# Kernel tuning notes

Measured on AMD Instinct MI355X. Metric: run time of the kernel, lower is better.

The kernel has to match this reference:

```python
import jax, jax.numpy as jnp
import numpy as np

B, T, E, H, C = 64, 512, 768, 128, 18


def setup_inputs() -> dict:
    key = jax.random.key(0)
    ks = jax.random.split(key, 16)
    s = 1.0 / np.sqrt(H)
    inp = {
        "x": jax.random.normal(ks[0], (B, T, E), jnp.float32),
        "attention_mask": jnp.ones((B, T), jnp.int32),
        "labels": jax.random.randint(ks[1], (B, T), 0, C, jnp.int32),
        "Wih_f": jax.random.uniform(ks[2], (4 * H, E), jnp.float32, -s, s),
        "Whh_f": jax.random.uniform(ks[3], (4 * H, H), jnp.float32, -s, s),
        "b_f": jax.random.uniform(ks[4], (4 * H,), jnp.float32, -s, s),
        "Wih_b": jax.random.uniform(ks[5], (4 * H, E), jnp.float32, -s, s),
        "Whh_b": jax.random.uniform(ks[6], (4 * H, H), jnp.float32, -s, s),
        "b_b": jax.random.uniform(ks[7], (4 * H,), jnp.float32, -s, s),
        "Wfc": jax.random.uniform(ks[8], (C, 2 * H), jnp.float32, -s, s),
        "bfc": jax.random.uniform(ks[9], (C,), jnp.float32, -s, s),
        "start_trans": jax.random.normal(ks[10], (C,), jnp.float32) * 0.1,
        "end_trans": jax.random.normal(ks[11], (C,), jnp.float32) * 0.1,
        "trans": jax.random.normal(ks[12], (C, C), jnp.float32) * 0.1,
    }
    return inp


def _lstm_dir(x, Wih, Whh, b, reverse=False):
    # x: [B, T, E] -> hidden states [B, T, H]; torch LSTM gate order i,f,g,o
    if reverse:
        x = x[:, ::-1]
    pre = jnp.einsum("bte,ge->btg", x, Wih) + b  # [B, T, 4H] input projection once
    h0 = jnp.zeros((x.shape[0], H), x.dtype)

    def step(carry, pt):
        h, c = carry
        g = pt + h @ Whh.T
        i, f, gg, o = jnp.split(g, 4, axis=-1)
        c = jax.nn.sigmoid(f) * c + jax.nn.sigmoid(i) * jnp.tanh(gg)
        h = jax.nn.sigmoid(o) * jnp.tanh(c)
        return (h, c), h

    _, hs = jax.lax.scan(step, (h0, h0), jnp.swapaxes(pre, 0, 1))
    hs = jnp.swapaxes(hs, 0, 1)
    if reverse:
        hs = hs[:, ::-1]
    return hs


def _crf_loglik(em, tags, mask, start, end, trans):
    # pytorch-crf log-likelihood, batch_first. em [B,T,C], tags/mask [B,T]
    b, t, _ = em.shape
    maskf = mask.astype(em.dtype)
    tags = tags.astype(jnp.int32)
    # numerator: score of the given tag path
    em_sc = jnp.take_along_axis(em, tags[..., None], axis=2)[..., 0]  # [B,T]
    num = start[tags[:, 0]] + em_sc[:, 0]
    num = num + jnp.sum(em_sc[:, 1:] * maskf[:, 1:], axis=1)
    num = num + jnp.sum(trans[tags[:, :-1], tags[:, 1:]] * maskf[:, 1:], axis=1)
    last_idx = jnp.sum(mask.astype(jnp.int32), axis=1) - 1
    last_tags = jnp.take_along_axis(tags, last_idx[:, None], axis=1)[:, 0]
    num = num + end[last_tags]
    # denominator: forward algorithm (logsumexp recurrence over time)
    alpha0 = start + em[:, 0]  # [B,C]

    def step(alpha, inp):
        e_t, m_t = inp
        new = jax.scipy.special.logsumexp(alpha[:, :, None] + trans[None], axis=1) + e_t
        return jnp.where(m_t[:, None], new, alpha), None

    alpha, _ = jax.lax.scan(
        step, alpha0,
        (jnp.swapaxes(em[:, 1:], 0, 1), jnp.swapaxes(mask[:, 1:].astype(bool), 0, 1)),
    )
    den = jax.scipy.special.logsumexp(alpha + end, axis=1)
    return num - den


def _viterbi(em, start, end, trans):
    # em [B,T,C] -> best path [B,T] (full mask)
    s0 = start + em[:, 0]

    def fstep(score, e_t):
        cand = score[:, :, None] + trans[None]  # [B,C,C]
        return jnp.max(cand, axis=1) + e_t, jnp.argmax(cand, axis=1)

    score, bptr = jax.lax.scan(fstep, s0, jnp.swapaxes(em[:, 1:], 0, 1))  # bptr [T-1,B,C]
    last = jnp.argmax(score + end, axis=1)  # [B]

    def bstep(tag, ptr_t):
        prev = jnp.take_along_axis(ptr_t, tag[:, None], axis=1)[:, 0]
        return prev, prev

    _, path = jax.lax.scan(bstep, last, bptr, reverse=True)  # [T-1,B]
    return jnp.concatenate([jnp.swapaxes(path, 0, 1), last[:, None]], axis=1)


def reference(x, attention_mask, labels, Wih_f, Whh_f, b_f, Wih_b, Whh_b, b_b,
              Wfc, bfc, start_trans, end_trans, trans):
    hf = _lstm_dir(x, Wih_f, Whh_f, b_f, reverse=False)
    hb = _lstm_dir(x, Wih_b, Whh_b, b_b, reverse=True)
    seq = jnp.concatenate([hf, hb], axis=-1)  # [B,T,2H]
    em = seq @ Wfc.T + bfc  # [B,T,C] emissions
    mask = attention_mask.astype(bool)
    llh = _crf_loglik(em, labels, mask, start_trans, end_trans, trans)
    loss = -jnp.sum(llh) / x.shape[0]  # reduction='sum' then / batch_size
    path = _viterbi(em, start_trans, end_trans, trans) + 1  # res_paths = x+1
    return path, loss
```

## Files before the change

### kernel.cpp

```cpp
#include <hip/hip_runtime.h>
#include <hip/hip_bf16.h>
#include <math.h>

typedef __attribute__((ext_vector_type(8))) short short8;
typedef __attribute__((ext_vector_type(4))) float f32x4;

constexpr int nB = 64, nT = 512, nE = 768, nH = 128, nG = 512, nC = 18;
constexpr int nBT = nB * nT;

__device__ __forceinline__ float bf2f(unsigned short u) { return __uint_as_float(((unsigned int)u) << 16); }
__device__ __forceinline__ unsigned short f2bf(float f) {
  __hip_bfloat16 h = __float2bfloat16(f);
  return *reinterpret_cast<unsigned short*>(&h);
}
__device__ __forceinline__ float rlane(float v, int lane) {
  return __uint_as_float(__builtin_amdgcn_readlane(__float_as_uint(v), lane));
}
__device__ __forceinline__ float fast_sig(float x) {
  return __builtin_amdgcn_rcpf(1.0f + __builtin_amdgcn_exp2f(-1.44269504f * x));
}
__device__ __forceinline__ float fast_tanh(float x) {
  return 1.0f - 2.0f * __builtin_amdgcn_rcpf(1.0f + __builtin_amdgcn_exp2f(2.88539008f * x));
}

__global__ __launch_bounds__(256) void cvt_kernel(const float* __restrict__ in,
                                                  unsigned short* __restrict__ out, int n8) {
  int i = blockIdx.x * blockDim.x + threadIdx.x;
  const int stride = gridDim.x * blockDim.x;
  for (; i < n8; i += stride) {
    const float4 a = ((const float4*)in)[(size_t)i * 2];
    const float4 b = ((const float4*)in)[(size_t)i * 2 + 1];
    unsigned short u[8] = {f2bf(a.x), f2bf(a.y), f2bf(a.z), f2bf(a.w),
                           f2bf(b.x), f2bf(b.y), f2bf(b.z), f2bf(b.w)};
    ((float4*)out)[i] = *(float4*)u;
  }
}

__global__ __launch_bounds__(256) void cvtw_kernel(const float* __restrict__ inF,
                                                   const float* __restrict__ inB,
                                                   unsigned short* __restrict__ outF,
                                                   unsigned short* __restrict__ outB, int n8) {
  const int half = gridDim.x >> 1;
  const float* in = (blockIdx.x < half) ? inF : inB;
  unsigned short* out = (blockIdx.x < half) ? outF : outB;
  const int bid = (blockIdx.x < half) ? blockIdx.x : blockIdx.x - half;
  int i = bid * blockDim.x + threadIdx.x;
  const int stride = half * blockDim.x;
  for (; i < n8; i += stride) {
    const float4 a = ((const float4*)in)[(size_t)i * 2];
    const float4 b = ((const float4*)in)[(size_t)i * 2 + 1];
    unsigned short u[8] = {f2bf(a.x), f2bf(a.y), f2bf(a.z), f2bf(a.w),
                           f2bf(b.x), f2bf(b.y), f2bf(b.z), f2bf(b.w)};
    ((float4*)out)[i] = *(float4*)u;
  }
}

__global__ __launch_bounds__(256) void proj_kernel(
    const unsigned short* __restrict__ xbf,
    const unsigned short* __restrict__ wfb, const unsigned short* __restrict__ wbb,
    const float* __restrict__ biasF, const float* __restrict__ biasB,
    unsigned short* __restrict__ Pf, unsigned short* __restrict__ Pb)
{
  const int bid = blockIdx.x;
  const int mt = bid & 255, sub = bid >> 8;
  const int dir = sub >> 2, nt = sub & 3;
  const unsigned short* W = dir ? wbb : wfb;
  const float* bias = dir ? biasB : biasF;
  unsigned short* P = dir ? Pb : Pf;
  const int m0 = mt * 128, n0 = nt * 128;

  __shared__ unsigned short As[128 * 40];
  __shared__ unsigned short Bs[128 * 40];
  const int tid = threadIdx.x;
  const int w = tid >> 6, lane = tid & 63, l15 = lane & 15, l4 = lane >> 4;
  const int wr = w >> 1, wc = w & 1;
  const int srow = tid >> 1, shalf = tid & 1;

  const unsigned short* srcA = xbf + (size_t)(m0 + srow) * nE + shalf * 16;
  const unsigned short* srcB = W + (size_t)(n0 + srow) * nE + shalf * 16;

  f32x4 acc[4][4];
#pragma unroll
  for (int i = 0; i < 4; ++i)
#pragma unroll
    for (int j = 0; j < 4; ++j) acc[i][j] = (f32x4){0.f, 0.f, 0.f, 0.f};

  for (int k0 = 0; k0 < nE; k0 += 32) {
    const float4 a0 = *(const float4*)(srcA + k0);
    const float4 a1 = *(const float4*)(srcA + k0 + 8);
    const float4 b0 = *(const float4*)(srcB + k0);
    const float4 b1 = *(const float4*)(srcB + k0 + 8);
    __syncthreads();
    *(float4*)&As[srow * 40 + shalf * 16] = a0;
    *(float4*)&As[srow * 40 + shalf * 16 + 8] = a1;
    *(float4*)&Bs[srow * 40 + shalf * 16] = b0;
    *(float4*)&Bs[srow * 40 + shalf * 16 + 8] = b1;
    __syncthreads();
    short8 af[4], bfr[4];
#pragma unroll
    for (int i = 0; i < 4; ++i) af[i] = *(const short8*)&As[(wr * 64 + i * 16 + l15) * 40 + l4 * 8];
#pragma unroll
    for (int j = 0; j < 4; ++j) bfr[j] = *(const short8*)&Bs[(wc * 64 + j * 16 + l15) * 40 + l4 * 8];
#pragma unroll
    for (int i = 0; i < 4; ++i)
#pragma unroll
      for (int j = 0; j < 4; ++j)
        acc[i][j] = __builtin_amdgcn_mfma_f32_16x16x32_bf16(af[i], bfr[j], acc[i][j], 0, 0, 0);
  }
  float bv[4];
#pragma unroll
  for (int j = 0; j < 4; ++j) bv[j] = bias[n0 + wc * 64 + j * 16 + l15];
#pragma unroll
  for (int i = 0; i < 4; ++i) {
#pragma unroll
    for (int j = 0; j < 4; ++j) {
      const int col = n0 + wc * 64 + j * 16 + l15;
#pragma unroll
      for (int r = 0; r < 4; ++r) {
        const int row = m0 + wr * 64 + i * 16 + l4 * 4 + r;
        P[(size_t)row * nG + col] = f2bf(acc[i][j][r] + bv[j]);
      }
    }
  }
}

__global__ __launch_bounds__(512, 1) void lstm_kernel(
    const unsigned short* __restrict__ Pf, const unsigned short* __restrict__ Pb,
    const float* __restrict__ WhhF, const float* __restrict__ WhhB,
    unsigned short* __restrict__ hf, unsigned short* __restrict__ hb)
{
  const int bid = blockIdx.x;
  const int dir = bid & 1, grp = bid >> 1;
  const int b0 = grp * 4;
  const unsigned short* pre = dir ? Pb : Pf;
  const float* Whh = dir ? WhhB : WhhF;
  unsigned short* hout = dir ? hb : hf;

  const int tid = threadIdx.x, w = tid >> 6, lane = tid & 63;
  const int l15 = lane & 15, l4 = lane >> 4;
  const int batch = l15 & 3, msel = l15 >> 2;
  const int cell = w * 16 + msel * 4 + l4;
  const int swz = batch * 40;

  __shared__ unsigned short h_lds[2 * 4 * 128];

  short8 Af[4][4];
#pragma unroll
  for (int m = 0; m < 4; ++m) {
    const int gp = w * 64 + m * 16 + l15;
    const int gorig = (gp & 3) * 128 + (gp >> 2);
#pragma unroll
    for (int kk = 0; kk < 4; ++kk) {
      const float* wp = Whh + (size_t)gorig * nH + kk * 32 + l4 * 8;
      const float4 v0 = *(const float4*)wp;
      const float4 v1 = *(const float4*)(wp + 4);
      unsigned short u[8] = {f2bf(v0.x), f2bf(v0.y), f2bf(v0.z), f2bf(v0.w),
                             f2bf(v1.x), f2bf(v1.y), f2bf(v1.z), f2bf(v1.w)};
      Af[m][kk] = *(short8*)u;
    }
  }
  for (int i = tid; i < 2 * 4 * 128; i += 512) h_lds[i] = 0;

  float c_state = 0.f;
  const unsigned short* pbase = pre + (size_t)(b0 + batch) * nT * nG + cell;

  unsigned short pA[4], pB[4];
  {
    const int tt0 = dir ? (nT - 1) : 0;
    const int tt1 = dir ? (nT - 2) : 1;
#pragma unroll
    for (int r = 0; r < 4; ++r) pA[r] = pbase[(size_t)tt0 * nG + r * 128];
#pragma unroll
    for (int r = 0; r < 4; ++r) pB[r] = pbase[(size_t)tt1 * nG + r * 128];
  }
  __syncthreads();

#define LSTM_STEP(RB, T, BUFC)                                                   \
  {                                                                              \
    const int ttime = dir ? (nT - 1 - (T)) : (T);                                \
    float pg[4];                                                                 \
    _Pragma("unroll")                                                            \
    for (int r = 0; r < 4; ++r) pg[r] = bf2f(BUFC[r]);                           \
    {                                                                            \
      const int tl = ((T) + 2 < nT) ? (T) + 2 : (T);                             \
      const int ttl = dir ? (nT - 1 - tl) : tl;                                  \
      _Pragma("unroll")                                                          \
      for (int r = 0; r < 4; ++r) BUFC[r] = pbase[(size_t)ttl * nG + r * 128];   \
    }                                                                            \
    short8 bfr[4];                                                               \
    _Pragma("unroll")                                                            \
    for (int kk = 0; kk < 4; ++kk) {                                             \
      const int idx = (RB) * 512 + batch * 128 + ((kk * 32 + l4 * 8) ^ swz);     \
      bfr[kk] = *(const short8*)&h_lds[idx];                                     \
    }                                                                            \
    f32x4 acc[4];                                                                \
    _Pragma("unroll")                                                            \
    for (int m = 0; m < 4; ++m) acc[m] = (f32x4){0.f, 0.f, 0.f, 0.f};            \
    _Pragma("unroll")                                                            \
    for (int kk = 0; kk < 4; ++kk)                                               \
      _Pragma("unroll")                                                          \
      for (int m = 0; m < 4; ++m)                                                \
        acc[m] = __builtin_amdgcn_mfma_f32_16x16x32_bf16(Af[m][kk], bfr[kk], acc[m], 0, 0, 0); \
    const float g0 = msel < 2 ? (msel == 0 ? acc[0][0] : acc[1][0]) : (msel == 2 ? acc[2][0] : acc[3][0]); \
    const float g1 = msel < 2 ? (msel == 0 ? acc[0][1] : acc[1][1]) : (msel == 2 ? acc[2][1] : acc[3][1]); \
    const float g2 = msel < 2 ? (msel == 0 ? acc[0][2] : acc[1][2]) : (msel == 2 ? acc[2][2] : acc[3][2]); \
    const float g3 = msel < 2 ? (msel == 0 ? acc[0][3] : acc[1][3]) : (msel == 2 ? acc[2][3] : acc[3][3]); \
    const float gi = g0 + pg[0], gf = g1 + pg[1], gg = g2 + pg[2], go = g3 + pg[3]; \
    c_state = fast_sig(gf) * c_state + fast_sig(gi) * fast_tanh(gg);             \
    const float hval = fast_sig(go) * fast_tanh(c_state);                        \
    const unsigned short hu = f2bf(hval);                                        \
    h_lds[((RB) ^ 1) * 512 + batch * 128 + (cell ^ swz)] = hu;                   \
    hout[((size_t)(b0 + batch) * nT + ttime) * nH + cell] = hu;                  \
    asm volatile("s_waitcnt lgkmcnt(0)" ::: "memory");                           \
    __builtin_amdgcn_sched_barrier(0);                                           \
    __builtin_amdgcn_s_barrier();                                                \
  }

  for (int t2 = 0; t2 < nT; t2 += 2) {
    LSTM_STEP(0, t2, pA)
    LSTM_STEP(1, t2 + 1, pB)
  }
#undef LSTM_STEP
}

__global__ __launch_bounds__(256) void em_kernel(
    const unsigned short* __restrict__ hf, const unsigned short* __restrict__ hb,
    const float* __restrict__ Wfc, const float* __restrict__ bfc,
    float* __restrict__ em)
{
  __shared__ float seq[32][260];
  __shared__ float Wf[18][260];
  const int tid = threadIdx.x;
  const int row0 = blockIdx.x * 32;
  for (int i = tid; i < 32 * 32; i += 256) {
    const int r = i >> 5, seg = i & 31;
    const unsigned short* src = (seg < 16) ? (hf + (size_t)(row0 + r) * nH + seg * 8)
                                           : (hb + (size_t)(row0 + r) * nH + (seg - 16) * 8);
    const float4 v = *(const float4*)src;
    const unsigned short* u = (const unsigned short*)&v;
#pragma unroll
    for (int k = 0; k < 8; ++k) seq[r][seg * 8 + k] = bf2f(u[k]);
  }
  for (int i = tid; i < nC * 256; i += 256) {
    const int cc = i >> 8, k = i & 255;
    Wf[cc][k] = Wfc[cc * 256 + k];
  }
  __syncthreads();
  for (int o = tid; o < 32 * nC; o += 256) {
    const int r = o / nC, cc = o - r * nC;
    float acc = bfc[cc];
    const float4* s4 = (const float4*)&seq[r][0];
    const float4* w4 = (const float4*)&Wf[cc][0];
#pragma unroll
    for (int q = 0; q < 64; ++q) {
      const float4 a = s4[q]; const float4 wv = w4[q];
      acc += a.x * wv.x + a.y * wv.y + a.z * wv.z + a.w * wv.w;
    }
    em[(size_t)(row0 + r) * nC + cc] = acc;
  }
}

__global__ __launch_bounds__(64) void crfvit_kernel(
    const float* __restrict__ em, const int* __restrict__ labels,
    const int* __restrict__ mask, const float* __restrict__ start,
    const float* __restrict__ endt, const float* __restrict__ trans,
    float* __restrict__ llh, float* __restrict__ out_path)
{
  constexpr float K2 = 1.44269504088896f;
  constexpr float LN2 = 0.69314718055995f;
  const int b = blockIdx.x >> 1, role = blockIdx.x & 1;
  const int l = threadIdx.x;
  __shared__ float tr[nC * nC];
  __shared__ unsigned char bp[(nT - 1) * nC];
  __shared__ unsigned char path[nT];
  for (int i = l; i < nC * nC; i += 64) tr[i] = trans[i];
  __syncthreads();
  const float* eb = em + (size_t)b * nT * nC;
  const int lc = l < nC ? l : nC - 1;

#define MAX18(c) fmaxf(fmaxf(fmaxf(fmaxf(fmaxf(c[0], c[1]), c[2]), fmaxf(fmaxf(c[3], c[4]), c[5])),           \
                             fmaxf(fmaxf(fmaxf(c[6], c[7]), c[8]), fmaxf(fmaxf(c[9], c[10]), c[11]))),        \
                       fmaxf(fmaxf(fmaxf(c[12], c[13]), c[14]), fmaxf(fmaxf(c[15], c[16]), c[17])))
#define TREESUM(ex, s) {                                                          \
    const float p0 = ex[0] + ex[1], p1 = ex[2] + ex[3], p2 = ex[4] + ex[5];       \
    const float p3 = ex[6] + ex[7], p4 = ex[8] + ex[9], p5 = ex[10] + ex[11];     \
    const float p6 = ex[12] + ex[13], p7 = ex[14] + ex[15], p8 = ex[16] + ex[17]; \
    const float q0 = p0 + p1, q1 = p2 + p3, q2 = p4 + p5, q3 = p6 + p7;           \
    s = ((q0 + q1) + (q2 + q3)) + p8;                                             \
  }

  if (role == 0) {
    const int* tg = labels + (size_t)b * nT;
    const int* mk = mask + (size_t)b * nT;

    float np = 0.f; int cnt = 0;
    for (int t = l; t < nT; t += 64) {
      const int tag = tg[t];
      const float e = eb[(size_t)t * nC + tag];
      if (t == 0) np += start[tag] + e;
      else np += (float)mk[t] * (e + tr[tg[t - 1] * nC + tag]);
      cnt += mk[t];
    }
#pragma unroll
    for (int off = 32; off; off >>= 1) { np += __shfl_xor(np, off); cnt += __shfl_xor(cnt, off); }
    const float num = np + endt[tg[cnt - 1]];

    float trc[nC];
#pragma unroll
    for (int i = 0; i < nC; ++i) trc[i] = tr[i * nC + lc] * K2;

    float alpha2 = (start[lc] + eb[lc]) * K2;
    float ec[8], en[8];
#pragma unroll
    for (int j = 0; j < 8; ++j) ec[j] = eb[j * nC + lc] * K2;
#pragma unroll
    for (int j = 0; j < 8; ++j) en[j] = eb[(8 + j) * nC + lc] * K2;
    unsigned long long mb = __ballot(mk[l] != 0);

#define CRF_STEP(T, E) {                                                          \
      float cand[nC];                                                             \
      _Pragma("unroll")                                                           \
      for (int i = 0; i < nC; ++i) cand[i] = rlane(alpha2, i) + trc[i];           \
      const float m = MAX18(cand);                                                \
      float ex[nC];                                                               \
      _Pragma("unroll")                                                           \
      for (int i = 0; i < nC; ++i) ex[i] = __builtin_amdgcn_exp2f(cand[i] - m);   \
      float s; TREESUM(ex, s);                                                    \
      const float anew = m + __builtin_amdgcn_logf(s) + (E);                      \
      alpha2 = ((mb >> ((T) & 63)) & 1) ? anew : alpha2;                          \
    }

#pragma unroll
    for (int j = 1; j < 8; ++j) CRF_STEP(j, ec[j])
    for (int c = 1; c < 64; ++c) {
#pragma unroll
      for (int j = 0; j < 8; ++j) ec[j] = en[j];
      const int tn = (c < 63) ? (c + 1) * 8 : 504;
#pragma unroll
      for (int j = 0; j < 8; ++j) en[j] = eb[(size_t)(tn + j) * nC + lc] * K2;
      if ((c & 7) == 0) mb = __ballot(mk[c * 8 + l] != 0);
#pragma unroll
      for (int j = 0; j < 8; ++j) CRF_STEP(c * 8 + j, ec[j])
    }
#undef CRF_STEP
    const float v = (l < nC) ? (alpha2 + endt[l] * K2) : -3.0e38f;
    float m = v;
#pragma unroll
    for (int off = 32; off; off >>= 1) m = fmaxf(m, __shfl_xor(m, off));
    float s = (l < nC) ? __builtin_amdgcn_exp2f(v - m) : 0.f;
#pragma unroll
    for (int off = 32; off; off >>= 1) s += __shfl_xor(s, off);
    if (l == 0) llh[b] = num - (m + __builtin_amdgcn_logf(s)) * LN2;
  } else {
    float trc[nC];
#pragma unroll
    for (int i = 0; i < nC; ++i) trc[i] = tr[i * nC + lc];

    float score_r = start[lc] + eb[lc];
    float ec[8], en[8];
#pragma unroll
    for (int j = 0; j < 8; ++j) ec[j] = eb[j * nC + lc];
#pragma unroll
    for (int j = 0; j < 8; ++j) en[j] = eb[(8 + j) * nC + lc];

#define VIT_STEP(T, E) {                                                          \
      float cand[nC];                                                             \
      _Pragma("unroll")                                                           \
      for (int i = 0; i < nC; ++i) cand[i] = rlane(score_r, i) + trc[i];          \
      const float m = MAX18(cand);                                                \
      int sel[nC];                                                                \
      _Pragma("unroll")                                                           \
      for (int i = 0; i < nC; ++i) sel[i] = (cand[i] == m) ? i : 63;              \
      int arg = sel[0];                                                           \
      _Pragma("unroll")                                                           \
      for (int i = 1; i < nC; ++i) arg = min(arg, sel[i]);                        \
      score_r = m + (E);                                                          \
      if (l < nC) bp[((T) - 1) * nC + l] = (unsigned char)arg;                    \
    }

#pragma unroll
    for (int j = 1; j < 8; ++j) VIT_STEP(j, ec[j])
    for (int c = 1; c < 64; ++c) {
#pragma unroll
      for (int j = 0; j < 8; ++j) ec[j] = en[j];
      const int tn = (c < 63) ? (c + 1) * 8 : 504;
#pragma unroll
      for (int j = 0; j < 8; ++j) en[j] = eb[(size_t)(tn + j) * nC + lc];
#pragma unroll
      for (int j = 0; j < 8; ++j) VIT_STEP(c * 8 + j, ec[j])
    }
#undef VIT_STEP
    if (l == 0) {
      float mm = -3.0e38f; int last = 0;
      for (int i = 0; i < nC; ++i) {
        const float v = rlane(score_r, i) + endt[i];
        if (v > mm) { mm = v; last = i; }
      }
      path[nT - 1] = (unsigned char)last;
      int cur = last;
      for (int t = nT - 2; t >= 0; --t) { cur = bp[t * nC + cur]; path[t] = (unsigned char)cur; }
    }
    asm volatile("s_waitcnt lgkmcnt(0)" ::: "memory");
    __builtin_amdgcn_wave_barrier();
    for (int t = l; t < nT; t += 64) out_path[(size_t)b * nT + t] = (float)(path[t] + 1);
  }
#undef MAX18
#undef TREESUM
}

__global__ __launch_bounds__(64) void loss_kernel(const float* __restrict__ llh, float* __restrict__ out)
{
  const int l = threadIdx.x;
  float v = llh[l];
#pragma unroll
  for (int off = 32; off; off >>= 1) v += __shfl_xor(v, off);
  if (l == 0) out[0] = -v / (float)nB;
}

extern "C" void kernel_launch(void* const* d_in, const int* in_sizes, int n_in,
                              void* d_out, int out_size, void* d_ws, size_t ws_size,
                              hipStream_t stream)
{
  const float* x      = (const float*)d_in[0];
  const int*   amask  = (const int*)d_in[1];
  const int*   labels = (const int*)d_in[2];
  const float* Wih_f  = (const float*)d_in[3];
  const float* Whh_f  = (const float*)d_in[4];
  const float* b_f    = (const float*)d_in[5];
  const float* Wih_b  = (const float*)d_in[6];
  const float* Whh_b  = (const float*)d_in[7];
  const float* b_b    = (const float*)d_in[8];
  const float* Wfc    = (const float*)d_in[9];
  const float* bfc    = (const float*)d_in[10];
  const float* start  = (const float*)d_in[11];
  const float* endt   = (const float*)d_in[12];
  const float* trans  = (const float*)d_in[13];

  float* out = (float*)d_out;
  float* ws = (float*)d_ws;
  unsigned short* preF = (unsigned short*)ws;
  unsigned short* preB = preF + (size_t)nBT * nG;
  unsigned short* hf   = preB + (size_t)nBT * nG;
  unsigned short* hb   = hf + (size_t)nBT * nH;
  float* em  = (float*)(hb + (size_t)nBT * nH);
  float* llh = em + (size_t)nBT * nC;
  unsigned short* xbf = (unsigned short*)(llh + 64);
  unsigned short* wfb = xbf + (size_t)nBT * nE;
  unsigned short* wbb = wfb + (size_t)nG * nE;

  cvt_kernel<<<4096, 256, 0, stream>>>(x, xbf, nBT * nE / 8);
  cvtw_kernel<<<384, 256, 0, stream>>>(Wih_f, Wih_b, wfb, wbb, nG * nE / 8);
  proj_kernel<<<2048, 256, 0, stream>>>(xbf, wfb, wbb, b_f, b_b, preF, preB);
  lstm_kernel<<<32, 512, 0, stream>>>(preF, preB, Whh_f, Whh_b, hf, hb);
  em_kernel<<<1024, 256, 0, stream>>>(hf, hb, Wfc, bfc, em);
  crfvit_kernel<<<128, 64, 0, stream>>>(em, labels, amask, start, endt, trans, llh, out);
  loss_kernel<<<1, 64, 0, stream>>>(llh, out + nBT);
}
```

Before: 542.4 us.

## Split LSTM into 2-batch blocks, merge convert kernels, use exp-domain CRF forward

```diff
diff --git a/kernel.cpp b/kernel.cpp
--- a/kernel.cpp
+++ b/kernel.cpp
@@ -22,30 +22,20 @@
 __device__ __forceinline__ float fast_tanh(float x) {
   return 1.0f - 2.0f * __builtin_amdgcn_rcpf(1.0f + __builtin_amdgcn_exp2f(2.88539008f * x));
 }
-
-__global__ __launch_bounds__(256) void cvt_kernel(const float* __restrict__ in,
-                                                  unsigned short* __restrict__ out, int n8) {
-  int i = blockIdx.x * blockDim.x + threadIdx.x;
-  const int stride = gridDim.x * blockDim.x;
-  for (; i < n8; i += stride) {
-    const float4 a = ((const float4*)in)[(size_t)i * 2];
-    const float4 b = ((const float4*)in)[(size_t)i * 2 + 1];
-    unsigned short u[8] = {f2bf(a.x), f2bf(a.y), f2bf(a.z), f2bf(a.w),
-                           f2bf(b.x), f2bf(b.y), f2bf(b.z), f2bf(b.w)};
-    ((float4*)out)[i] = *(float4*)u;
-  }
-}
-
-__global__ __launch_bounds__(256) void cvtw_kernel(const float* __restrict__ inF,
-                                                   const float* __restrict__ inB,
-                                                   unsigned short* __restrict__ outF,
-                                                   unsigned short* __restrict__ outB, int n8) {
-  const int half = gridDim.x >> 1;
-  const float* in = (blockIdx.x < half) ? inF : inB;
-  unsigned short* out = (blockIdx.x < half) ? outF : outB;
-  const int bid = (blockIdx.x < half) ? blockIdx.x : blockIdx.x - half;
-  int i = bid * blockDim.x + threadIdx.x;
-  const int stride = half * blockDim.x;
+__device__ __forceinline__ float max3h(float a, float b, float c) { return fmaxf(fmaxf(a, b), c); }
+
+__global__ __launch_bounds__(256) void cvt_all(const float* __restrict__ x,
+                                               const float* __restrict__ wF,
+                                               const float* __restrict__ wB,
+                                               unsigned short* __restrict__ xo,
+                                               unsigned short* __restrict__ wFo,
+                                               unsigned short* __restrict__ wBo) {
+  const float* in; unsigned short* out; int n8, bid, nblk;
+  if (blockIdx.x < 4096)      { in = x;  out = xo;  n8 = nBT * nE / 8; bid = blockIdx.x;        nblk = 4096; }
+  else if (blockIdx.x < 4288) { in = wF; out = wFo; n8 = nG * nE / 8;  bid = blockIdx.x - 4096; nblk = 192; }
+  else                        { in = wB; out = wBo; n8 = nG * nE / 8;  bid = blockIdx.x - 4288; nblk = 192; }
+  int i = bid * 256 + threadIdx.x;
+  const int stride = nblk * 256;
   for (; i < n8; i += stride) {
     const float4 a = ((const float4*)in)[(size_t)i * 2];
     const float4 b = ((const float4*)in)[(size_t)i * 2 + 1];
@@ -124,30 +114,29 @@
   }
 }
 
-__global__ __launch_bounds__(512, 1) void lstm_kernel(
+__global__ __launch_bounds__(256, 1) void lstm_kernel(
     const unsigned short* __restrict__ Pf, const unsigned short* __restrict__ Pb,
     const float* __restrict__ WhhF, const float* __restrict__ WhhB,
     unsigned short* __restrict__ hf, unsigned short* __restrict__ hb)
 {
   const int bid = blockIdx.x;
-  const int dir = bid & 1, grp = bid >> 1;
-  const int b0 = grp * 4;
+  const int dir = bid & 1, pair = bid >> 1;
+  const int b0 = pair * 2;
   const unsigned short* pre = dir ? Pb : Pf;
   const float* Whh = dir ? WhhB : WhhF;
   unsigned short* hout = dir ? hb : hf;
 
   const int tid = threadIdx.x, w = tid >> 6, lane = tid & 63;
   const int l15 = lane & 15, l4 = lane >> 4;
-  const int batch = l15 & 3, msel = l15 >> 2;
-  const int cell = w * 16 + msel * 4 + l4;
-  const int swz = batch * 40;
-
-  __shared__ unsigned short h_lds[2 * 4 * 128];
-
-  short8 Af[4][4];
-#pragma unroll
-  for (int m = 0; m < 4; ++m) {
-    const int gp = w * 64 + m * 16 + l15;
+  const int batch = l15 & 1, msel = l15 >> 1;
+  const int cell = w * 32 + msel * 4 + l4;
+
+  __shared__ unsigned short h_lds[2 * 2 * 128];
+
+  short8 Af[8][4];
+#pragma unroll
+  for (int m = 0; m < 8; ++m) {
+    const int gp = w * 128 + m * 16 + l15;
     const int gorig = (gp & 3) * 128 + (gp >> 2);
 #pragma unroll
     for (int kk = 0; kk < 4; ++kk) {
@@ -159,7 +148,7 @@
       Af[m][kk] = *(short8*)u;
     }
   }
-  for (int i = tid; i < 2 * 4 * 128; i += 512) h_lds[i] = 0;
+  for (int i = tid; i < 2 * 2 * 128; i += 256) h_lds[i] = 0;
 
   float c_state = 0.f;
   const unsigned short* pbase = pre + (size_t)(b0 + batch) * nT * nG + cell;
@@ -189,27 +178,28 @@
     }                                                                            \
     short8 bfr[4];                                                               \
     _Pragma("unroll")                                                            \
-    for (int kk = 0; kk < 4; ++kk) {                                             \
-      const int idx = (RB) * 512 + batch * 128 + ((kk * 32 + l4 * 8) ^ swz);     \
-      bfr[kk] = *(const short8*)&h_lds[idx];                                     \
-    }                                                                            \
-    f32x4 acc[4];                                                                \
+    for (int kk = 0; kk < 4; ++kk)                                               \
+      bfr[kk] = *(const short8*)&h_lds[(RB) * 256 + batch * 128 + kk * 32 + l4 * 8]; \
+    f32x4 acc[8];                                                                \
     _Pragma("unroll")                                                            \
-    for (int m = 0; m < 4; ++m) acc[m] = (f32x4){0.f, 0.f, 0.f, 0.f};            \
+    for (int m = 0; m < 8; ++m) acc[m] = (f32x4){0.f, 0.f, 0.f, 0.f};            \
     _Pragma("unroll")                                                            \
     for (int kk = 0; kk < 4; ++kk)                                               \
       _Pragma("unroll")                                                          \
-      for (int m = 0; m < 4; ++m)                                                \
+      for (int m = 0; m < 8; ++m)                                                \
         acc[m] = __builtin_amdgcn_mfma_f32_16x16x32_bf16(Af[m][kk], bfr[kk], acc[m], 0, 0, 0); \
-    const float g0 = msel < 2 ? (msel == 0 ? acc[0][0] : acc[1][0]) : (msel == 2 ? acc[2][0] : acc[3][0]); \
-    const float g1 = msel < 2 ? (msel == 0 ? acc[0][1] : acc[1][1]) : (msel == 2 ? acc[2][1] : acc[3][1]); \
-    const float g2 = msel < 2 ? (msel == 0 ? acc[0][2] : acc[1][2]) : (msel == 2 ? acc[2][2] : acc[3][2]); \
-    const float g3 = msel < 2 ? (msel == 0 ? acc[0][3] : acc[1][3]) : (msel == 2 ? acc[2][3] : acc[3][3]); \
-    const float gi = g0 + pg[0], gf = g1 + pg[1], gg = g2 + pg[2], go = g3 + pg[3]; \
+    const f32x4 t0 = (msel & 1) ? acc[1] : acc[0];                               \
+    const f32x4 t1 = (msel & 1) ? acc[3] : acc[2];                               \
+    const f32x4 t2 = (msel & 1) ? acc[5] : acc[4];                               \
+    const f32x4 t3 = (msel & 1) ? acc[7] : acc[6];                               \
+    const f32x4 u0 = (msel & 2) ? t1 : t0;                                       \
+    const f32x4 u1 = (msel & 2) ? t3 : t2;                                       \
+    const f32x4 g = (msel & 4) ? u1 : u0;                                        \
+    const float gi = g[0] + pg[0], gf = g[1] + pg[1], gg = g[2] + pg[2], go = g[3] + pg[3]; \
     c_state = fast_sig(gf) * c_state + fast_sig(gi) * fast_tanh(gg);             \
     const float hval = fast_sig(go) * fast_tanh(c_state);                        \
     const unsigned short hu = f2bf(hval);                                        \
-    h_lds[((RB) ^ 1) * 512 + batch * 128 + (cell ^ swz)] = hu;                   \
+    h_lds[((RB) ^ 1) * 256 + batch * 128 + cell] = hu;                           \
     hout[((size_t)(b0 + batch) * nT + ttime) * nH + cell] = hu;                  \
     asm volatile("s_waitcnt lgkmcnt(0)" ::: "memory");                           \
     __builtin_amdgcn_sched_barrier(0);                                           \
@@ -278,16 +268,8 @@
   const float* eb = em + (size_t)b * nT * nC;
   const int lc = l < nC ? l : nC - 1;
 
-#define MAX18(c) fmaxf(fmaxf(fmaxf(fmaxf(fmaxf(c[0], c[1]), c[2]), fmaxf(fmaxf(c[3], c[4]), c[5])),           \
-                             fmaxf(fmaxf(fmaxf(c[6], c[7]), c[8]), fmaxf(fmaxf(c[9], c[10]), c[11]))),        \
-                       fmaxf(fmaxf(fmaxf(c[12], c[13]), c[14]), fmaxf(fmaxf(c[15], c[16]), c[17])))
-#define TREESUM(ex, s) {                                                          \
-    const float p0 = ex[0] + ex[1], p1 = ex[2] + ex[3], p2 = ex[4] + ex[5];       \
-    const float p3 = ex[6] + ex[7], p4 = ex[8] + ex[9], p5 = ex[10] + ex[11];     \
-    const float p6 = ex[12] + ex[13], p7 = ex[14] + ex[15], p8 = ex[16] + ex[17]; \
-    const float q0 = p0 + p1, q1 = p2 + p3, q2 = p4 + p5, q3 = p6 + p7;           \
-    s = ((q0 + q1) + (q2 + q3)) + p8;                                             \
-  }
+#define MAX18T(c) fmaxf(max3h(max3h(c[0], c[1], c[2]), max3h(c[3], c[4], c[5]), max3h(c[6], c[7], c[8])),     \
+                        max3h(max3h(c[9], c[10], c[11]), max3h(c[12], c[13], c[14]), max3h(c[15], c[16], c[17])))
 
   if (role == 0) {
     const int* tg = labels + (size_t)b * nT;
@@ -305,9 +287,9 @@
     for (int off = 32; off; off >>= 1) { np += __shfl_xor(np, off); cnt += __shfl_xor(cnt, off); }
     const float num = np + endt[tg[cnt - 1]];
 
-    float trc[nC];
-#pragma unroll
-    for (int i = 0; i < nC; ++i) trc[i] = tr[i * nC + lc] * K2;
+    float M2[nC];
+#pragma unroll
+    for (int i = 0; i < nC; ++i) M2[i] = __builtin_amdgcn_exp2f(tr[i * nC + lc] * K2);
 
     float alpha2 = (start[lc] + eb[lc]) * K2;
     float ec[8], en[8];
@@ -318,15 +300,19 @@
     unsigned long long mb = __ballot(mk[l] != 0);
 
 #define CRF_STEP(T, E) {                                                          \
-      float cand[nC];                                                             \
+      float A2 = alpha2;                                                          \
+      A2 = fmaxf(A2, __shfl_xor(A2, 32)); A2 = fmaxf(A2, __shfl_xor(A2, 16));     \
+      A2 = fmaxf(A2, __shfl_xor(A2, 8));  A2 = fmaxf(A2, __shfl_xor(A2, 4));      \
+      A2 = fmaxf(A2, __shfl_xor(A2, 2));  A2 = fmaxf(A2, __shfl_xor(A2, 1));      \
+      const float vv = __builtin_amdgcn_exp2f(alpha2 - A2);                       \
+      float s0 = 0.f, s1 = 0.f, s2 = 0.f;                                         \
       _Pragma("unroll")                                                           \
-      for (int i = 0; i < nC; ++i) cand[i] = rlane(alpha2, i) + trc[i];           \
-      const float m = MAX18(cand);                                                \
-      float ex[nC];                                                               \
-      _Pragma("unroll")                                                           \
-      for (int i = 0; i < nC; ++i) ex[i] = __builtin_amdgcn_exp2f(cand[i] - m);   \
-      float s; TREESUM(ex, s);                                                    \
-      const float anew = m + __builtin_amdgcn_logf(s) + (E);                      \
+      for (int i = 0; i < nC; i += 3) {                                           \
+        s0 = fmaf(rlane(vv, i), M2[i], s0);                                       \
+        s1 = fmaf(rlane(vv, i + 1), M2[i + 1], s1);                               \
+        s2 = fmaf(rlane(vv, i + 2), M2[i + 2], s2);                               \
+      }                                                                           \
+      const float anew = A2 + __builtin_amdgcn_logf((s0 + s1) + s2) + (E);        \
       alpha2 = ((mb >> ((T) & 63)) & 1) ? anew : alpha2;                          \
     }
 
@@ -367,7 +353,7 @@
       float cand[nC];                                                             \
       _Pragma("unroll")                                                           \
       for (int i = 0; i < nC; ++i) cand[i] = rlane(score_r, i) + trc[i];          \
-      const float m = MAX18(cand);                                                \
+      const float m = MAX18T(cand);                                               \
       int sel[nC];                                                                \
       _Pragma("unroll")                                                           \
       for (int i = 0; i < nC; ++i) sel[i] = (cand[i] == m) ? i : 63;              \
@@ -404,8 +390,7 @@
     __builtin_amdgcn_wave_barrier();
     for (int t = l; t < nT; t += 64) out_path[(size_t)b * nT + t] = (float)(path[t] + 1);
   }
-#undef MAX18
-#undef TREESUM
+#undef MAX18T
 }
 
 __global__ __launch_bounds__(64) void loss_kernel(const float* __restrict__ llh, float* __restrict__ out)
@@ -448,10 +433,9 @@
   unsigned short* wfb = xbf + (size_t)nBT * nE;
   unsigned short* wbb = wfb + (size_t)nG * nE;
 
-  cvt_kernel<<<4096, 256, 0, stream>>>(x, xbf, nBT * nE / 8);
-  cvtw_kernel<<<384, 256, 0, stream>>>(Wih_f, Wih_b, wfb, wbb, nG * nE / 8);
+  cvt_all<<<4480, 256, 0, stream>>>(x, Wih_f, Wih_b, xbf, wfb, wbb);
   proj_kernel<<<2048, 256, 0, stream>>>(xbf, wfb, wbb, b_f, b_b, preF, preB);
-  lstm_kernel<<<32, 512, 0, stream>>>(preF, preB, Whh_f, Whh_b, hf, hb);
+  lstm_kernel<<<64, 256, 0, stream>>>(preF, preB, Whh_f, Whh_b, hf, hb);
   em_kernel<<<1024, 256, 0, stream>>>(hf, hb, Wfc, bfc, em);
   crfvit_kernel<<<128, 64, 0, stream>>>(em, labels, amask, start, endt, trans, llh, out);
   loss_kernel<<<1, 64, 0, stream>>>(llh, out + nBT);
```

Result: slower. 562.6 us, median of 3 (+3.7%).
